# Performance work log

Measured on AMD Instinct MI355X. Metric: run time of the kernel, lower is better.

## Reference

```python
import jax, jax.numpy as jnp
import numpy as np

B, N, C, K = 8, 4096, 128, 20  # batch, points-per-cloud, channels (n_cout), knn neighbors
NEG_SLOPE = 0.01  # torch F.leaky_relu default


def setup_inputs() -> dict:
    key = jax.random.key(0)
    ks = jax.random.split(key, 6)
    s = 1.0 / np.sqrt(C).astype(np.float32)
    xyz = jax.random.normal(ks[0], (B, 3, N), jnp.float32)
    points = jax.random.normal(ks[1], (B, C, N), jnp.float32)
    Wc = jax.random.normal(ks[2], (C, C), jnp.float32) * s  # center 1x1 conv weight (out,in)
    bc = jax.random.normal(ks[3], (C,), jnp.float32) * s
    Wg = jax.random.normal(ks[4], (C, C), jnp.float32) * s  # grouped 1x1 conv weight
    bg = jax.random.normal(ks[5], (C,), jnp.float32) * s
    return {"xyz": xyz, "points": points, "Wc": Wc, "bc": bc, "Wg": Wg, "bg": bg}


def reference(xyz, points, Wc, bc, Wg, bg):
    # xyz: [B,3,N], points: [B,C,N]
    k = K
    shortcut = points
    p = jax.nn.leaky_relu(points, NEG_SLOPE)        # [B,C,N]
    pt = jnp.transpose(p, (0, 2, 1))                # [B,N,C]
    xt = jnp.transpose(xyz, (0, 2, 1))              # [B,N,3]

    # pairwise squared distances [B,N,N]
    sq_norm = jnp.sum(xt * xt, axis=-1)             # [B,N]
    sq = sq_norm[:, :, None] - 2.0 * jnp.einsum('bnd,bmd->bnm', xt, xt) + sq_norm[:, None, :]

    # knn: k+1 nearest (incl. self), drop self -> [B,N,k]
    _, idx = jax.lax.top_k(-sq, k + 1)
    idx = idx[:, :, 1:]

    # gather neighbor features: [B,N,k,C]
    grouped = jax.vmap(lambda a, i: a[i])(pt, idx)

    # center 1x1 conv on [B,C,1,N] == per-point linear
    center = jnp.einsum('oc,bcn->bon', Wc, p) + bc[None, :, None]      # [B,C,N]
    # grouped 1x1 conv on [B,C,k,N]
    gout = jnp.einsum('oc,bnkc->bokn', Wg, grouped) + bg[None, :, None, None]  # [B,C,k,N]

    # mean over concat([center(1), grouped(k)], axis=2) then residual
    pooled = (center + jnp.sum(gout, axis=2)) / (k + 1)
    return pooled + shortcut
```

## Files before the change

kernel.cpp:

```cpp
#include <hip/hip_runtime.h>

#define B 8
#define N 4096
#define C 128
#define C2 256
#define KNN 21
#define CAP 12

typedef unsigned long long u64;
typedef unsigned int u32;
typedef unsigned short u16;

typedef __attribute__((ext_vector_type(8))) short bf16x8;
typedef __attribute__((ext_vector_type(4))) float f32x4;

__device__ __forceinline__ float bf2f(u16 u) {
    return __uint_as_float(((u32)u) << 16);
}
__device__ __forceinline__ u16 f2bf(float f) {
    u32 x = __float_as_uint(f);
    return (u16)((x + 0x7FFFu + ((x >> 16) & 1u)) >> 16);
}

__global__ __launch_bounds__(256) void k_transpose_lrelu(
        const float* __restrict__ pts, u16* __restrict__ X) {
    __shared__ u16 tile[32][33];
    int b  = blockIdx.z;
    int c0 = blockIdx.y * 32;
    int n0 = blockIdx.x * 32;
    int tx = threadIdx.x, ty = threadIdx.y;
    const float* src = pts + (size_t)b * C * N;
    #pragma unroll
    for (int i = 0; i < 32; i += 8) {
        float v = src[(size_t)(c0 + ty + i) * N + n0 + tx];
        if (v < 0.f) v = __fmul_rn(v, 0.01f);
        tile[ty + i][tx] = f2bf(v);
    }
    __syncthreads();
    u16* dst = X + (size_t)b * N * C2;
    #pragma unroll
    for (int i = 0; i < 32; i += 8) {
        dst[(size_t)(n0 + ty + i) * C2 + (c0 + tx)] = tile[tx][ty + i];
    }
}

__global__ __launch_bounds__(256) void k_knn_gather(
        const float* __restrict__ xyz, u16* __restrict__ X) {
    __shared__ __align__(16) char lds[34816];
    float4* stg  = (float4*)lds;
    u32*    kbuf = (u32*)(lds + 16384);
    u16*    ibuf = (u16*)(lds + 16384 + 12288);
    u32*    mk   = (u32*)lds;
    u16*    mi   = (u16*)(lds + 21504);
    __shared__ u16 win[32 * KNN];

    int tid = threadIdx.x;
    int w = tid >> 6, l = tid & 63;
    int q = l >> 1, h = l & 1;
    int b = blockIdx.y;
    int n0 = blockIdx.x * 32;
    int nq = n0 + q;

    const float* xz = xyz + (size_t)b * 3 * N;
    float qx = xz[nq], qy = xz[N + nq], qz = xz[2 * N + nq];
    float snq = __fadd_rn(__fadd_rn(__fmul_rn(qx, qx), __fmul_rn(qy, qy)),
                          __fmul_rn(qz, qz));

    u32 key[KNN], idx[KNN];
    #pragma unroll
    for (int i = 0; i < KNN; ++i) { key[i] = 0xFFFFFFFFu; idx[i] = 0u; }
    int cnt = 0;
    u32 thr = 0xFFFFFFFFu;

    auto compact = [&]() {
        #pragma unroll 1
        for (int i = 0; i < CAP; ++i) {
            if (__ballot(i < cnt) == 0ull) break;
            u32 kv = kbuf[i * 256 + tid];
            u32 iv = ibuf[i * 256 + tid];
            bool ins = (i < cnt) && (kv < key[20]);
            if (__ballot(ins) != 0ull) {
                key[20] = ins ? kv : key[20];
                idx[20] = ins ? iv : idx[20];
                #pragma unroll
                for (int t = 19; t >= 0; --t) {
                    bool sw = key[t] > key[t + 1];
                    u32 ka = sw ? key[t + 1] : key[t];
                    u32 kz = sw ? key[t] : key[t + 1];
                    u32 ia = sw ? idx[t + 1] : idx[t];
                    u32 iz = sw ? idx[t] : idx[t + 1];
                    key[t] = ka; key[t + 1] = kz;
                    idx[t] = ia; idx[t + 1] = iz;
                }
            }
        }
        cnt = 0;
        thr = key[20];
    };

    for (int sc = 0; sc < 4; ++sc) {
        #pragma unroll
        for (int r = 0; r < 4; ++r) {
            int e = l + 64 * r;
            int he = e >> 7, je = e & 127;
            int m = w * 1024 + he * 512 + sc * 128 + je;
            float x = xz[m], y = xz[N + m], z = xz[2 * N + m];
            float sn = __fadd_rn(__fadd_rn(__fmul_rn(x, x), __fmul_rn(y, y)),
                                 __fmul_rn(z, z));
            stg[w * 256 + e] = make_float4(x, y, z, sn);
        }
        asm volatile("s_waitcnt lgkmcnt(0)" ::: "memory");
        int mbase = w * 1024 + h * 512 + sc * 128;
        const float4* mystg = stg + w * 256 + h * 128;
        for (int cc = 0; cc < 128; cc += 4) {
            #pragma unroll
            for (int u = 0; u < 4; ++u) {
                float4 cp = mystg[cc + u];
                int m = mbase + cc + u;
                float dot = __fadd_rn(__fadd_rn(__fmul_rn(qx, cp.x),
                                                __fmul_rn(qy, cp.y)),
                                      __fmul_rn(qz, cp.z));
                float sq = __fadd_rn(__fsub_rn(snq, __fadd_rn(dot, dot)), cp.w);
                u32 bits = __float_as_uint(sq);
                u32 kb = bits ^ (0x80000000u | (u32)(((int)bits) >> 31));
                kbuf[cnt * 256 + tid] = kb;
                ibuf[cnt * 256 + tid] = (u16)m;
                cnt += (kb < thr);
            }
            if (__ballot(cnt > 8) != 0ull) compact();
        }
    }
    compact();

    __syncthreads();
    #pragma unroll
    for (int j = 0; j < KNN; ++j) {
        mk[(w * 64 + l) * KNN + j] = key[j];
        mi[(w * 64 + l) * KNN + j] = idx[j];
    }
    __syncthreads();

    if (w == 0 && l < 32) {
        int p[1];
        int p0 = 0, p1 = 0, p2 = 0, p3 = 0, p4 = 0, p5 = 0, p6 = 0, p7 = 0;
        (void)p;
        #pragma unroll 1
        for (int j = 0; j < KNN; ++j) {
            #define LOADC(r, pr) \
                u64 c##r = ((u64)mk[(((r) >> 1) * 64 + l * 2 + ((r) & 1)) * KNN + pr] << 16) \
                         |  (u64)mi[(((r) >> 1) * 64 + l * 2 + ((r) & 1)) * KNN + pr];
            LOADC(0, p0) LOADC(1, p1) LOADC(2, p2) LOADC(3, p3)
            LOADC(4, p4) LOADC(5, p5) LOADC(6, p6) LOADC(7, p7)
            #undef LOADC
            u64 m01 = c0 < c1 ? c0 : c1; int s01 = c0 < c1 ? 0 : 1;
            u64 m23 = c2 < c3 ? c2 : c3; int s23 = c2 < c3 ? 2 : 3;
            u64 m45 = c4 < c5 ? c4 : c5; int s45 = c4 < c5 ? 4 : 5;
            u64 m67 = c6 < c7 ? c6 : c7; int s67 = c6 < c7 ? 6 : 7;
            u64 m03 = m01 < m23 ? m01 : m23; int s03 = m01 < m23 ? s01 : s23;
            u64 m47 = m45 < m67 ? m45 : m67; int s47 = m45 < m67 ? s45 : s67;
            u64 mm  = m03 < m47 ? m03 : m47; int sel = m03 < m47 ? s03 : s47;
            win[l * KNN + j] = (u16)(mm & 0xFFFFu);
            p0 += (sel == 0); p1 += (sel == 1); p2 += (sel == 2); p3 += (sel == 3);
            p4 += (sel == 4); p5 += (sel == 5); p6 += (sel == 6); p7 += (sel == 7);
        }
    }
    __syncthreads();

    const u16* Xb = X + (size_t)b * N * C2;
    for (int qq = 0; qq < 8; ++qq) {
        int qg = w * 8 + qq;
        float f0 = 0.f, f1 = 0.f;
        #pragma unroll
        for (int j = 1; j < KNN; ++j) {
            int m = win[qg * KNN + j];
            u32 u2 = *(const u32*)(Xb + (size_t)m * C2 + 2 * l);
            f0 += bf2f((u16)(u2 & 0xFFFFu));
            f1 += bf2f((u16)(u2 >> 16));
        }
        u16* dst = X + ((size_t)b * N + n0 + qg) * C2 + 128 + 2 * l;
        *(u32*)dst = ((u32)f2bf(f1) << 16) | (u32)f2bf(f0);
    }
}

__global__ __launch_bounds__(256) void k_gemm_mfma(
        const u16* __restrict__ X, const float* __restrict__ Wc,
        const float* __restrict__ Wg, const float* __restrict__ pts,
        const float* __restrict__ bc, const float* __restrict__ bg,
        float* __restrict__ out) {
    int wid = blockIdx.x * 4 + (threadIdx.x >> 6);
    int lane = threadIdx.x & 63;
    int ot = wid & 7;
    int nt = wid >> 3;
    int b  = nt >> 6;
    int n0 = (nt & 63) * 64;

    int l16 = lane & 15, lq = lane >> 4;
    const u16* Xb = X + (size_t)b * N * C2;
    const u16* bptr0 = Xb + (size_t)(n0 + 0 * 16 + l16) * C2 + lq * 8;
    const u16* bptr1 = Xb + (size_t)(n0 + 1 * 16 + l16) * C2 + lq * 8;
    const u16* bptr2 = Xb + (size_t)(n0 + 2 * 16 + l16) * C2 + lq * 8;
    const u16* bptr3 = Xb + (size_t)(n0 + 3 * 16 + l16) * C2 + lq * 8;
    const float* wrowc = Wc + (size_t)(ot * 16 + l16) * 128 + lq * 8;
    const float* wrowg = Wg + (size_t)(ot * 16 + l16) * 128 + lq * 8;

    f32x4 acc0 = {0.f, 0.f, 0.f, 0.f};
    f32x4 acc1 = {0.f, 0.f, 0.f, 0.f};
    f32x4 acc2 = {0.f, 0.f, 0.f, 0.f};
    f32x4 acc3 = {0.f, 0.f, 0.f, 0.f};
    #pragma unroll
    for (int kk = 0; kk < 8; ++kk) {
        const float* ws = (kk < 4) ? (wrowc + kk * 32) : (wrowg + (kk - 4) * 32);
        float4 wa = *(const float4*)ws;
        float4 wb = *(const float4*)(ws + 4);
        bf16x8 a;
        a[0] = (short)f2bf(wa.x); a[1] = (short)f2bf(wa.y);
        a[2] = (short)f2bf(wa.z); a[3] = (short)f2bf(wa.w);
        a[4] = (short)f2bf(wb.x); a[5] = (short)f2bf(wb.y);
        a[6] = (short)f2bf(wb.z); a[7] = (short)f2bf(wb.w);
        bf16x8 b0 = *(const bf16x8*)(bptr0 + kk * 32);
        bf16x8 b1 = *(const bf16x8*)(bptr1 + kk * 32);
        bf16x8 b2 = *(const bf16x8*)(bptr2 + kk * 32);
        bf16x8 b3 = *(const bf16x8*)(bptr3 + kk * 32);
        acc0 = __builtin_amdgcn_mfma_f32_16x16x32_bf16(a, b0, acc0, 0, 0, 0);
        acc1 = __builtin_amdgcn_mfma_f32_16x16x32_bf16(a, b1, acc1, 0, 0, 0);
        acc2 = __builtin_amdgcn_mfma_f32_16x16x32_bf16(a, b2, acc2, 0, 0, 0);
        acc3 = __builtin_amdgcn_mfma_f32_16x16x32_bf16(a, b3, acc3, 0, 0, 0);
    }

    const float inv21 = 1.0f / 21.0f;
    float bias[4];
    #pragma unroll
    for (int r = 0; r < 4; ++r) {
        int o = ot * 16 + lq * 4 + r;
        bias[r] = bc[o] + 20.f * bg[o];
    }
    const float* pb = pts + (size_t)b * C * N;
    float* ob = out + (size_t)b * C * N;
    f32x4 accs[4] = {acc0, acc1, acc2, acc3};
    #pragma unroll
    for (int t = 0; t < 4; ++t) {
        int n = n0 + t * 16 + l16;
        #pragma unroll
        for (int r = 0; r < 4; ++r) {
            int o = ot * 16 + lq * 4 + r;
            ob[(size_t)o * N + n] =
                (accs[t][r] + bias[r]) * inv21 + pb[(size_t)o * N + n];
        }
    }
}

extern "C" void kernel_launch(void* const* d_in, const int* in_sizes, int n_in,
                              void* d_out, int out_size, void* d_ws, size_t ws_size,
                              hipStream_t stream) {
    const float* xyz = (const float*)d_in[0];
    const float* pts = (const float*)d_in[1];
    const float* Wc  = (const float*)d_in[2];
    const float* bc  = (const float*)d_in[3];
    const float* Wg  = (const float*)d_in[4];
    const float* bg  = (const float*)d_in[5];
    float* out = (float*)d_out;

    u16* X = (u16*)d_ws;

    k_transpose_lrelu<<<dim3(N / 32, C / 32, B), dim3(32, 8), 0, stream>>>(pts, X);
    k_knn_gather<<<dim3(N / 32, B), dim3(256), 0, stream>>>(xyz, X);
    k_gemm_mfma<<<dim3(1024), dim3(256), 0, stream>>>(X, Wc, Wg, pts, bc, bg, out);
}
```

Measured before the change: 321.6 us.

## Replace threshold-buffered top-k with branchless sorting-network merge per 8 candidates

The per-thread top-21 selection no longer buffers candidates that pass a threshold in LDS and periodically compacts them with an insertion pass. Instead, each group of 8 candidates is sorted with a fixed 19-comparator network and bitonic-merged with the running 21-element sorted list held as packed 64-bit key/index values. This removes LDS traffic, ballots and divergent compaction, and frees LDS. The cost is a fixed set of 64-bit compare-swaps for every batch, even when no candidate would qualify, plus higher register pressure from 29 u64 values.

```diff
diff --git a/kernel.cpp b/kernel.cpp
--- a/kernel.cpp
+++ b/kernel.cpp
@@ -5,7 +5,6 @@
 #define C 128
 #define C2 256
 #define KNN 21
-#define CAP 12
 
 typedef unsigned long long u64;
 typedef unsigned int u32;
@@ -46,12 +45,10 @@
 
 __global__ __launch_bounds__(256) void k_knn_gather(
         const float* __restrict__ xyz, u16* __restrict__ X) {
-    __shared__ __align__(16) char lds[34816];
-    float4* stg  = (float4*)lds;
-    u32*    kbuf = (u32*)(lds + 16384);
-    u16*    ibuf = (u16*)(lds + 16384 + 12288);
-    u32*    mk   = (u32*)lds;
-    u16*    mi   = (u16*)(lds + 21504);
+    __shared__ __align__(16) char lds[32256];
+    float4* stg = (float4*)lds;
+    u32*    mk  = (u32*)lds;
+    u16*    mi  = (u16*)(lds + 21504);
     __shared__ u16 win[32 * KNN];
 
     int tid = threadIdx.x;
@@ -66,37 +63,9 @@
     float snq = __fadd_rn(__fadd_rn(__fmul_rn(qx, qx), __fmul_rn(qy, qy)),
                           __fmul_rn(qz, qz));
 
-    u32 key[KNN], idx[KNN];
-    #pragma unroll
-    for (int i = 0; i < KNN; ++i) { key[i] = 0xFFFFFFFFu; idx[i] = 0u; }
-    int cnt = 0;
-    u32 thr = 0xFFFFFFFFu;
-
-    auto compact = [&]() {
-        #pragma unroll 1
-        for (int i = 0; i < CAP; ++i) {
-            if (__ballot(i < cnt) == 0ull) break;
-            u32 kv = kbuf[i * 256 + tid];
-            u32 iv = ibuf[i * 256 + tid];
-            bool ins = (i < cnt) && (kv < key[20]);
-            if (__ballot(ins) != 0ull) {
-                key[20] = ins ? kv : key[20];
-                idx[20] = ins ? iv : idx[20];
-                #pragma unroll
-                for (int t = 19; t >= 0; --t) {
-                    bool sw = key[t] > key[t + 1];
-                    u32 ka = sw ? key[t + 1] : key[t];
-                    u32 kz = sw ? key[t] : key[t + 1];
-                    u32 ia = sw ? idx[t + 1] : idx[t];
-                    u32 iz = sw ? idx[t] : idx[t + 1];
-                    key[t] = ka; key[t + 1] = kz;
-                    idx[t] = ia; idx[t + 1] = iz;
-                }
-            }
-        }
-        cnt = 0;
-        thr = key[20];
-    };
+    u64 k[KNN];
+    #pragma unroll
+    for (int i = 0; i < KNN; ++i) k[i] = ~0ull;
 
     for (int sc = 0; sc < 4; ++sc) {
         #pragma unroll
@@ -112,9 +81,11 @@
         asm volatile("s_waitcnt lgkmcnt(0)" ::: "memory");
         int mbase = w * 1024 + h * 512 + sc * 128;
         const float4* mystg = stg + w * 256 + h * 128;
-        for (int cc = 0; cc < 128; cc += 4) {
-            #pragma unroll
-            for (int u = 0; u < 4; ++u) {
+        #pragma unroll 1
+        for (int cc = 0; cc < 128; cc += 8) {
+            u64 c[8];
+            #pragma unroll
+            for (int u = 0; u < 8; ++u) {
                 float4 cp = mystg[cc + u];
                 int m = mbase + cc + u;
                 float dot = __fadd_rn(__fadd_rn(__fmul_rn(qx, cp.x),
@@ -123,27 +94,51 @@
                 float sq = __fadd_rn(__fsub_rn(snq, __fadd_rn(dot, dot)), cp.w);
                 u32 bits = __float_as_uint(sq);
                 u32 kb = bits ^ (0x80000000u | (u32)(((int)bits) >> 31));
-                kbuf[cnt * 256 + tid] = kb;
-                ibuf[cnt * 256 + tid] = (u16)m;
-                cnt += (kb < thr);
+                c[u] = ((u64)kb << 32) | (u32)m;
             }
-            if (__ballot(cnt > 8) != 0ull) compact();
-        }
-    }
-    compact();
+            #define CS(i, j) { u64 _a = c[i], _b = c[j]; bool _t = _a < _b; \
+                               c[i] = _t ? _a : _b; c[j] = _t ? _b : _a; }
+            CS(0,1) CS(2,3) CS(4,5) CS(6,7)
+            CS(0,2) CS(1,3) CS(4,6) CS(5,7)
+            CS(1,2) CS(5,6)
+            CS(0,4) CS(1,5) CS(2,6) CS(3,7)
+            CS(2,4) CS(3,5)
+            CS(1,2) CS(3,4) CS(5,6)
+            #undef CS
+            u64 v[29];
+            #pragma unroll
+            for (int i = 0; i < 8; ++i) v[i] = c[7 - i];
+            #pragma unroll
+            for (int i = 0; i < KNN; ++i) v[8 + i] = k[i];
+            #define CE(i, j) { u64 _a = v[i], _b = v[j]; bool _t = _a < _b; \
+                               v[i] = _t ? _a : _b; v[j] = _t ? _b : _a; }
+            CE(0,16) CE(1,17) CE(2,18) CE(3,19) CE(4,20) CE(5,21) CE(6,22)
+            CE(7,23) CE(8,24) CE(9,25) CE(10,26) CE(11,27) CE(12,28)
+            CE(0,8) CE(1,9) CE(2,10) CE(3,11) CE(4,12) CE(5,13) CE(6,14) CE(7,15)
+            CE(16,24) CE(17,25) CE(18,26) CE(19,27) CE(20,28)
+            CE(0,4) CE(1,5) CE(2,6) CE(3,7)
+            CE(8,12) CE(9,13) CE(10,14) CE(11,15)
+            CE(16,20) CE(17,21) CE(18,22) CE(19,23)
+            CE(0,2) CE(1,3) CE(4,6) CE(5,7) CE(8,10) CE(9,11)
+            CE(12,14) CE(13,15) CE(16,18) CE(17,19) CE(20,22) CE(21,23)
+            CE(0,1) CE(2,3) CE(4,5) CE(6,7) CE(8,9) CE(10,11)
+            CE(12,13) CE(14,15) CE(16,17) CE(18,19) CE(20,21)
+            #undef CE
+            #pragma unroll
+            for (int i = 0; i < KNN; ++i) k[i] = v[i];
+        }
+    }
 
     __syncthreads();
     #pragma unroll
     for (int j = 0; j < KNN; ++j) {
-        mk[(w * 64 + l) * KNN + j] = key[j];
-        mi[(w * 64 + l) * KNN + j] = idx[j];
+        mk[(w * 64 + l) * KNN + j] = (u32)(k[j] >> 32);
+        mi[(w * 64 + l) * KNN + j] = (u16)(k[j] & 0xFFFFu);
     }
     __syncthreads();
 
     if (w == 0 && l < 32) {
-        int p[1];
         int p0 = 0, p1 = 0, p2 = 0, p3 = 0, p4 = 0, p5 = 0, p6 = 0, p7 = 0;
-        (void)p;
         #pragma unroll 1
         for (int j = 0; j < KNN; ++j) {
             #define LOADC(r, pr) \
```

After: 351.7 us. 9.4% more time.
